# Optimization experiments

Measured on AMD Instinct MI355X. Metric: run time of the kernel, lower is better.

## Reference

```python
import jax, jax.numpy as jnp
import numpy as np


def _lstm_bi(x, wih, whh, b):
    # x: [B,T,D]; wih: [2,D,4H]; whh: [2,H,4H]; b: [2,4H]. PyTorch gate order i,f,g,o.
    def run(xs, wi, wh, bb):
        B, H = xs.shape[1], wh.shape[0]
        def step(carry, xt):
            h, c = carry
            g = xt @ wi + h @ wh + bb
            i, f, gg, o = jnp.split(g, 4, axis=-1)
            c = jax.nn.sigmoid(f) * c + jax.nn.sigmoid(i) * jnp.tanh(gg)
            h = jax.nn.sigmoid(o) * jnp.tanh(c)
            return (h, c), h
        z0 = jnp.zeros((B, H), xs.dtype)
        _, hs = jax.lax.scan(step, (z0, z0), xs)
        return hs
    xs = jnp.swapaxes(x, 0, 1)  # [T,B,D]
    hf = run(xs, wih[0], whh[0], b[0])
    hb = run(xs[::-1], wih[1], whh[1], b[1])[::-1]
    return jnp.swapaxes(jnp.concatenate([hf, hb], axis=-1), 0, 1)


def _norm_thr(att, thr):
    # sum-normalize, threshold-sparsify, renormalize (PSP core)
    att = att / (jnp.sum(att, -1, keepdims=True) + 1e-8)
    att = jnp.where(att > thr, att, jnp.zeros_like(att))
    return att / (jnp.sum(att, -1, keepdims=True) + 1e-8)


def _ln(x, g, b):
    mu = jnp.mean(x, -1, keepdims=True)
    var = jnp.mean(jnp.square(x - mu), -1, keepdims=True)
    return (x - mu) / jnp.sqrt(var + 1e-6) * g + b


def _forward(audio, video, thr_val, fa_w1, fa_w2, av_aw, av_ab, av_vw, av_vb,
             av_v2w, av_gw, av_hw, fv_w1, fv_w2, la_wih, la_whh, la_b,
             lv_wih, lv_whh, lv_b, vL1, vL2, aL1, aL2, vfc, afc, ln_g, ln_b, L1w, L2w):
    bs, T = audio.shape[0], audio.shape[1]
    fa = (audio @ fa_w1) @ fa_w2                          # [B,T,128]
    vf = video.reshape(bs, T, -1, video.shape[-1])        # [B,T,49,512]
    # AVGA audio-guided visual attention
    v_h = jax.nn.relu(vf @ av_vw + av_vb)                 # [B,T,49,512]
    a_h = jax.nn.relu(fa @ av_aw + av_ab)                 # [B,T,512]
    content = v_h @ av_v2w + (a_h @ av_gw)[..., None]     # [B,T,49,49]
    z = jnp.squeeze(jnp.tanh(content) @ av_hw, -1)        # [B,T,49]
    alpha = jax.nn.softmax(z, -1)
    video_t = jnp.einsum('btp,btpd->btd', alpha, vf)      # [B,T,512]
    video_t = (video_t @ fv_w1) @ fv_w2                   # [B,T,128]
    # bidirectional LSTMs
    lstm_a = _lstm_bi(fa, la_wih, la_whh, la_b)           # [B,T,256]
    lstm_v = _lstm_bi(video_t, lv_wih, lv_whh, lv_b)      # [B,T,256]
    # PSP (eval mode: dropout is identity)
    v_b1 = jax.nn.relu(lstm_v @ vL1)
    v_b2 = jax.nn.relu(lstm_v @ vL2)
    a_b1 = jax.nn.relu(lstm_a @ aL1)
    a_b2 = jax.nn.relu(lstm_a @ aL2)
    scale = 1.0 / jnp.sqrt(jnp.asarray(v_b2.shape[-1], v_b2.dtype))
    att = jax.nn.relu(jnp.einsum('bvd,bad->bva', v_b2, a_b1) * scale)  # v->a raw
    att_v2a = _norm_thr(att, thr_val)
    att_a2v = _norm_thr(jnp.swapaxes(att, 1, 2), thr_val)
    v_psp = lstm_v + jnp.einsum('bva,bad->bvd', att_v2a, a_b2)
    a_psp = lstm_a + jnp.einsum('bav,bvd->bad', att_a2v, v_b1)
    v_psp = _ln(jax.nn.relu(v_psp @ vfc), ln_g, ln_b)
    a_psp = _ln(jax.nn.relu(a_psp @ afc), ln_g, ln_b)
    fuse = 0.5 * (v_psp + a_psp)
    vn = v_psp / jnp.maximum(jnp.linalg.norm(v_psp, axis=-1, keepdims=True), 1e-12)
    an = a_psp / jnp.maximum(jnp.linalg.norm(a_psp, axis=-1, keepdims=True), 1e-12)
    cross_att = jnp.sum(vn * an, -1)                      # [B,T]
    out = jax.nn.relu(fuse @ L1w) @ L2w                   # [B,T,29]
    return (fuse, out, cross_att)


def setup_inputs() -> dict:
    key = jax.random.key(0)
    ks = iter(jax.random.split(key, 40))
    def w(*shape):
        fan_in = shape[-2] if len(shape) > 1 else shape[-1]
        return jax.random.normal(next(ks), shape, jnp.float32) * (1.0 / np.sqrt(fan_in))
    B, T = 256, 10
    return dict(
        audio=jax.random.normal(next(ks), (B, T, 128), jnp.float32),
        video=jax.random.normal(next(ks), (B, T, 7, 7, 512), jnp.float32),
        thr_val=jnp.float32(0.099),
        fa_w1=w(128, 256), fa_w2=w(256, 128),
        av_aw=w(128, 512), av_ab=jnp.zeros((512,), jnp.float32),
        av_vw=w(512, 512), av_vb=jnp.zeros((512,), jnp.float32),
        av_v2w=w(512, 49), av_gw=w(512, 49), av_hw=w(49, 1),
        fv_w1=w(512, 256), fv_w2=w(256, 128),
        la_wih=w(2, 128, 512), la_whh=w(2, 128, 512), la_b=jnp.zeros((2, 512), jnp.float32),
        lv_wih=w(2, 128, 512), lv_whh=w(2, 128, 512), lv_b=jnp.zeros((2, 512), jnp.float32),
        vL1=w(256, 256), vL2=w(256, 256), aL1=w(256, 256), aL2=w(256, 256),
        vfc=w(256, 256), afc=w(256, 256),
        ln_g=jnp.ones((256,), jnp.float32), ln_b=jnp.zeros((256,), jnp.float32),
        L1w=w(256, 64), L2w=w(64, 29),
    )


def reference(audio, video, thr_val, fa_w1, fa_w2, av_aw, av_ab, av_vw, av_vb,
              av_v2w, av_gw, av_hw, fv_w1, fv_w2, la_wih, la_whh, la_b,
              lv_wih, lv_whh, lv_b, vL1, vL2, aL1, aL2, vfc, afc, ln_g, ln_b, L1w, L2w):
    return _forward(audio, video, thr_val, fa_w1, fa_w2, av_aw, av_ab, av_vw, av_vb,
                    av_v2w, av_gw, av_hw, fv_w1, fv_w2, la_wih, la_whh, la_b,
                    lv_wih, lv_whh, lv_b, vL1, vL2, aL1, aL2, vfc, afc, ln_g, ln_b, L1w, L2w)
```

## Files before the change

### kernel.cpp

```cpp
#include <hip/hip_runtime.h>
#include <math.h>

#define DEV __device__ __forceinline__

typedef _Float16 f16x8 __attribute__((ext_vector_type(8)));
typedef _Float16 f16x4 __attribute__((ext_vector_type(4)));
typedef float    f32x4 __attribute__((ext_vector_type(4)));

DEV float sigmoidf_(float x){ return 1.0f/(1.0f + expf(-x)); }

DEV float wred64(float x){
    #pragma unroll
    for (int off=32; off; off>>=1) x += __shfl_xor(x, off);
    return x;
}

#define MFMA16(a,b,c) __builtin_amdgcn_mfma_f32_16x16x32_f16(a,b,c,0,0,0)

DEV void packone(const float* __restrict__ src, int N, int NfrTot, int nfOff,
                 _Float16* __restrict__ Dh, _Float16* __restrict__ Dl, int o){
    int j = o&7, l16 = (o>>3)&15, kg = (o>>7)&3;
    int rest = o>>9;
    int nfl = rest % (N>>4), kt = rest / (N>>4);
    int k = kt*32 + kg*8 + j, n = nfl*16 + l16;
    float x = src[(size_t)k*N + n];
    _Float16 h = (_Float16)x;
    size_t d = ((size_t)kt*NfrTot + nfOff + nfl)*512 + kg*128 + l16*8 + j;
    Dh[d] = h; Dl[d] = (_Float16)(x - (float)h);
}

__global__ __launch_bounds__(256) void k_prep(
    const float* __restrict__ fa_w1, const float* __restrict__ fa_w2, float* __restrict__ faW,
    const float* __restrict__ fv_w1, const float* __restrict__ fv_w2,
    const float* __restrict__ av_vw, _Float16* __restrict__ Bh, _Float16* __restrict__ Bl,
    const float* __restrict__ v2w, _Float16* __restrict__ Wh, _Float16* __restrict__ Wl,
    const float* __restrict__ lv_wih,
    _Float16* __restrict__ PKfv_h, _Float16* __restrict__ PKfv_l,
    _Float16* __restrict__ PKxv_h, _Float16* __restrict__ PKxv_l)
{
    int bid = blockIdx.x, t = threadIdx.x;
    if (bid < 64){
        int idx = bid*256+t; int m = idx>>7, n = idx&127;
        float acc=0.f;
        for (int k=0;k<256;k++) acc += fa_w1[m*256+k]*fa_w2[k*128+n];
        faW[idx]=acc;
    } else if (bid < 1088){
        int o = (bid-64)*256+t;
        int j = o & 7, l16 = (o>>3)&15, kg = (o>>7)&3, nf = (o>>9)&31, kt = o>>14;
        int k = kt*32 + kg*8 + j, n = nf*16 + l16;
        float x = av_vw[(size_t)k*512 + n];
        _Float16 h = (_Float16)x;
        Bh[o] = h; Bl[o] = (_Float16)(x - (float)h);
    } else if (bid < 1216){
        int o = (bid-1088)*256+t;
        int j = o & 7, l16 = (o>>3)&15, kg = (o>>7)&3, qf = (o>>9)&3, kbg = o>>11;
        int k = kbg*32 + kg*8 + j, q = qf*16 + l16;
        float x = (q < 49) ? v2w[(size_t)k*49 + q] : 0.f;
        _Float16 h = (_Float16)x;
        Wh[o] = h; Wl[o] = (_Float16)(x - (float)h);
    } else if (bid < 1472){
        int o = (bid-1216)*256+t;
        int j=o&7, l16=(o>>3)&15, kg=(o>>7)&3; int rest=o>>9;
        int nfl = rest&7, kt = rest>>3;
        int k = kt*32+kg*8+j, n = nfl*16+l16;
        float acc=0.f;
        for (int kk=0;kk<256;kk++) acc += fv_w1[k*256+kk]*fv_w2[kk*128+n];
        _Float16 h=(_Float16)acc;
        size_t d = ((size_t)kt*8 + nfl)*512 + kg*128 + l16*8 + j;
        PKfv_h[d]=h; PKfv_l[d]=(_Float16)(acc-(float)h);
    } else {
        int seg = (bid-1472)>>8;
        int o = ((bid-1472)&255)*256+t;
        packone(lv_wih + (size_t)seg*65536, 512, 64, seg*32, PKxv_h, PKxv_l, o);
    }
}

__global__ __launch_bounds__(512) void k_faga2(
    const float* __restrict__ audio, const float* __restrict__ faW,
    const float* __restrict__ av_aw, const float* __restrict__ av_ab,
    const float* __restrict__ av_gw,
    const float* __restrict__ la_wih, const float* __restrict__ la_b,
    float* __restrict__ gGA, float* __restrict__ xpA)
{
    int b0 = blockIdx.x*8; int tid = threadIdx.x;
    __shared__ float sau[8][128], sfa[8][128], sah[8][512];
    for (int i=tid;i<1024;i+=512){ int bt=i>>7,k=i&127; sau[bt][k]=audio[(size_t)(b0+bt)*128+k]; }
    __syncthreads();
    for (int u=0;u<2;u++){
        int i=tid+u*512, bt=i>>7, n=i&127;
        float acc=0.f;
        for (int k4=0;k4<32;k4++){
            float4 x4=*(const float4*)&sau[bt][k4*4];
            acc+=x4.x*faW[(k4*4)*128+n]+x4.y*faW[(k4*4+1)*128+n]
                +x4.z*faW[(k4*4+2)*128+n]+x4.w*faW[(k4*4+3)*128+n];
        }
        sfa[bt][n]=acc;
    }
    __syncthreads();
    {
        int n=tid;
        float bv=av_ab[n];
        float acc[8]={bv,bv,bv,bv,bv,bv,bv,bv};
        for (int k4=0;k4<32;k4++){
            float w0=av_aw[(k4*4)*512+n], w1=av_aw[(k4*4+1)*512+n],
                  w2=av_aw[(k4*4+2)*512+n], w3=av_aw[(k4*4+3)*512+n];
            #pragma unroll
            for (int bt=0;bt<8;bt++){
                float4 x4=*(const float4*)&sfa[bt][k4*4];
                acc[bt]+=x4.x*w0+x4.y*w1+x4.z*w2+x4.w*w3;
            }
        }
        #pragma unroll
        for (int bt=0;bt<8;bt++) sah[bt][n]=fmaxf(acc[bt],0.f);
    }
    __syncthreads();
    if (tid<392){
        int bt=tid/49, q=tid%49;
        float acc=0.f;
        for (int k=0;k<512;k++) acc+=sah[bt][k]*av_gw[k*49+q];
        gGA[(size_t)(b0+bt)*49+q]=acc;
    }
    for (int u=0;u<2;u++){
        int n = tid + u*512;
        int dir = n >> 9, g = n & 511;
        const float* W = la_wih + (size_t)dir*65536;
        float bvv = la_b[dir*512 + g];
        float acc[8] = {bvv,bvv,bvv,bvv,bvv,bvv,bvv,bvv};
        for (int k4=0;k4<32;k4++){
            float w0=W[(k4*4+0)*512+g], w1=W[(k4*4+1)*512+g],
                  w2=W[(k4*4+2)*512+g], w3=W[(k4*4+3)*512+g];
            #pragma unroll
            for (int bt=0;bt<8;bt++){
                float4 x4=*(const float4*)&sfa[bt][k4*4];
                acc[bt]+=x4.x*w0+x4.y*w1+x4.z*w2+x4.w*w3;
            }
        }
        #pragma unroll
        for (int bt=0;bt<8;bt++)
            xpA[((size_t)(b0+bt))*1024 + n] = acc[bt];
    }
}

DEV void cvt4_(float4 v, f16x4& hv, f16x4& lv){
    hv[0]=(_Float16)v.x; lv[0]=(_Float16)(v.x-(float)hv[0]);
    hv[1]=(_Float16)v.y; lv[1]=(_Float16)(v.y-(float)hv[1]);
    hv[2]=(_Float16)v.z; lv[2]=(_Float16)(v.z-(float)hv[2]);
    hv[3]=(_Float16)v.w; lv[3]=(_Float16)(v.w-(float)hv[3]);
}

__global__ __launch_bounds__(256,2) void k_avga_fused(
    const float* __restrict__ video,
    const _Float16* __restrict__ Bh, const _Float16* __restrict__ Bl,
    const float* __restrict__ bias,
    const _Float16* __restrict__ Wh, const _Float16* __restrict__ Wl,
    const float* __restrict__ gGA, const float* __restrict__ hw,
    float* __restrict__ vT)
{
    __shared__ __align__(16) char smem[67072];
    int bt = blockIdx.x;
    int t = threadIdx.x;
    int lane = t & 63, w = t >> 6;
    int l16 = lane & 15, lq = lane >> 4;
    int lb = lane * 16;

    int am = t >> 3, ak = (t & 7) * 4;
    int aoff1 = ((am>>4)*4 + (ak>>3))*256 + (am&15)*16 + (ak&7)*2;
    int am2 = am + 32;
    int aoff2 = ((am2>>4)*4 + (ak>>3))*256 + (am2&15)*16 + (ak&7)*2;
    size_t r1 = (size_t)bt*49 + am;  if (r1 > 125439) r1 = 125439;
    size_t r2 = (size_t)bt*49 + am2; if (r2 > 125439) r2 = 125439;
    const float* Arow1 = video + r1*512 + ak;
    const float* Arow2 = video + r2*512 + ak;

    const f32x4 vzero = {0.f,0.f,0.f,0.f};
    f32x4 acc[4][8];
    #pragma unroll
    for (int p=0;p<4;p++)
        #pragma unroll
        for (int q=0;q<8;q++) acc[p][q] = vzero;

    float4 pa0, pa1;
    pa0 = *(const float4*)(Arow1);
    pa1 = *(const float4*)(Arow2);
    {
        f16x4 hv, lv;
        char* h = &smem[0];
        cvt4_(pa0, hv, lv);
        *(f16x4*)(h + aoff1) = hv; *(f16x4*)(h + 4096 + aoff1) = lv;
        cvt4_(pa1, hv, lv);
        *(f16x4*)(h + aoff2) = hv; *(f16x4*)(h + 4096 + aoff2) = lv;
    }
    __syncthreads();

    for (int kt = 0; kt < 16; ++kt){
        int cur = kt & 1;
        bool more = (kt < 15);
        if (more){
            pa0 = *(const float4*)(Arow1 + (kt+1)*32);
            pa1 = *(const float4*)(Arow2 + (kt+1)*32);
        }
        const char* aB = &smem[cur*8192];
        f16x8 ah[4], al[4];
        #pragma unroll
        for (int p=0;p<4;p++){
            ah[p] = *(const f16x8*)(aB + p*1024 + lb);
            al[p] = *(const f16x8*)(aB + 4096 + p*1024 + lb);
        }
        #pragma unroll
        for (int q=0;q<8;q++){
            size_t bo = (size_t)kt*16384 + (size_t)(w*8 + q)*512 + lane*8;
            f16x8 bh  = *(const f16x8*)(Bh + bo);
            f16x8 bl2 = *(const f16x8*)(Bl + bo);
            #pragma unroll
            for (int p=0;p<4;p++){
                acc[p][q] = MFMA16(ah[p], bh,  acc[p][q]);
                acc[p][q] = MFMA16(ah[p], bl2, acc[p][q]);
                acc[p][q] = MFMA16(al[p], bh,  acc[p][q]);
            }
        }
        if (more){
            char* h = &smem[(cur^1)*8192];
            f16x4 hv, lv;
            cvt4_(pa0, hv, lv);
            *(f16x4*)(h + aoff1) = hv; *(f16x4*)(h + 4096 + aoff1) = lv;
            cvt4_(pa1, hv, lv);
            *(f16x4*)(h + aoff2) = hv; *(f16x4*)(h + 4096 + aoff2) = lv;
        }
        __syncthreads();
    }

    float bv[8];
    #pragma unroll
    for (int q=0;q<8;q++) bv[q] = bias[w*128 + q*16 + l16];

    char* vh = &smem[16384 + w*8192];
    f32x4 cacc[4][4];
    #pragma unroll
    for (int p=0;p<4;p++)
        #pragma unroll
        for (int qf=0;qf<4;qf++) cacc[p][qf] = vzero;

    #pragma unroll
    for (int c=0;c<4;c++){
        #pragma unroll
        for (int p=0;p<4;p++)
            #pragma unroll
            for (int qq=0;qq<2;qq++){
                int q = c*2 + qq;
                int offbase = p*1024 + (qq*2 + (l16>>3))*256 + (l16&7)*2;
                #pragma unroll
                for (int r=0;r<4;r++){
                    float x = fmaxf(acc[p][q][r] + bv[q], 0.f);
                    _Float16 hh = (_Float16)x;
                    _Float16 ll = (_Float16)(x - (float)hh);
                    int off = offbase + (lq*4 + r)*16;
                    *(_Float16*)(vh + off)        = hh;
                    *(_Float16*)(vh + 4096 + off) = ll;
                }
            }
        int kbg = w*4 + c;
        f16x8 vhh[4], vhl[4];
        #pragma unroll
        for (int p=0;p<4;p++){
            vhh[p] = *(const f16x8*)(vh + p*1024 + lb);
            vhl[p] = *(const f16x8*)(vh + 4096 + p*1024 + lb);
        }
        #pragma unroll
        for (int qf=0;qf<4;qf++){
            size_t wo = (size_t)kbg*2048 + qf*512 + lane*8;
            f16x8 wh = *(const f16x8*)(Wh + wo);
            f16x8 wl = *(const f16x8*)(Wl + wo);
            #pragma unroll
            for (int p=0;p<4;p++){
                cacc[p][qf] = MFMA16(vhh[p], wh, cacc[p][qf]);
                cacc[p][qf] = MFMA16(vhh[p], wl, cacc[p][qf]);
                cacc[p][qf] = MFMA16(vhl[p], wh, cacc[p][qf]);
            }
        }
    }

    __syncthreads();
    float* pw = (float*)&smem[w*16384];
    #pragma unroll
    for (int p=0;p<4;p++)
        #pragma unroll
        for (int qf=0;qf<4;qf++)
            #pragma unroll
            for (int r=0;r<4;r++)
                pw[(p*16 + lq*4 + r)*64 + qf*16 + l16] = cacc[p][qf][r];
    __syncthreads();
    float* cb = (float*)&smem[0];
    for (int i=t; i<4096; i+=256)
        cb[i] = cb[i] + cb[4096+i] + cb[8192+i] + cb[12288+i];
    __syncthreads();

    float* szp    = (float*)&smem[65536];
    float* salpha = (float*)&smem[66560];
    if (t < 196){
        int p = t >> 2, ds = t & 3;
        float ga = gGA[(size_t)bt*49 + p];
        float part = 0.f;
        for (int q = ds*13; q < ds*13+13 && q < 49; q++)
            part += tanhf(cb[p*64 + q] + ga) * hw[q];
        szp[t] = part;
    }
    __syncthreads();
    if (t < 64){
        float z = (t<49) ? (szp[t*4]+szp[t*4+1]+szp[t*4+2]+szp[t*4+3]) : -1e30f;
        float m = z;
        #pragma unroll
        for (int off=32; off; off>>=1) m = fmaxf(m, __shfl_xor(m, off));
        float e = (t<49)? expf(z - m) : 0.f;
        float s = e;
        #pragma unroll
        for (int off=32; off; off>>=1) s += __shfl_xor(s, off);
        salpha[t] = e / s;
    }
    __syncthreads();
    const float* vb = video + (size_t)bt*49*512;
    #pragma unroll
    for (int u=0;u<2;u++){
        int d = t + u*256;
        float a0 = 0.f;
        for (int p=0;p<49;p++) a0 += salpha[p] * vb[(size_t)p*512 + d];
        vT[(size_t)bt*512 + d] = a0;
    }
}

__global__ __launch_bounds__(256) void k_gemm2(
    const float* __restrict__ vT,
    const _Float16* __restrict__ Fh, const _Float16* __restrict__ Fl,
    const _Float16* __restrict__ Xh, const _Float16* __restrict__ Xl,
    const float* __restrict__ lv_b,
    float* __restrict__ xpV)
{
    __shared__ __align__(16) char sA[2][4096];
    __shared__ float sV[32][132];
    int t = threadIdx.x, lane = t&63, w = t>>6;
    int l16 = lane&15, lq = lane>>4, lb = lane*16;
    int row0 = blockIdx.x * 32;

    int am = t>>3, ak = (t&7)*4;
    int aoff = ((am>>4)*4 + (ak>>3))*256 + (am&15)*16 + (ak&7)*2;
    const float* Arow = vT + (size_t)(row0+am)*512 + ak;

    const f32x4 vzero = {0.f,0.f,0.f,0.f};
    f32x4 acc1[2][2];
    #pragma unroll
    for (int p=0;p<2;p++)
        #pragma unroll
        for (int q=0;q<2;q++) acc1[p][q] = vzero;

    float4 pa = *(const float4*)(Arow);
    {
        f16x4 hv, lv;
        char* h = &sA[0][0];
        cvt4_(pa, hv, lv);
        *(f16x4*)(h + aoff) = hv; *(f16x4*)(h + 2048 + aoff) = lv;
    }
    __syncthreads();
    for (int kt = 0; kt < 16; ++kt){
        int cur = kt & 1;
        bool more = (kt < 15);
        if (more) pa = *(const float4*)(Arow + (kt+1)*32);
        const char* aB = &sA[cur][0];
        f16x8 ah[2], al[2];
        #pragma unroll
        for (int p=0;p<2;p++){
            ah[p] = *(const f16x8*)(aB + p*1024 + lb);
            al[p] = *(const f16x8*)(aB + 2048 + p*1024 + lb);
        }
        #pragma unroll
        for (int q=0;q<2;q++){
            size_t bo = ((size_t)kt*8 + w*2 + q)*512 + lane*8;
            f16x8 bh  = *(const f16x8*)(Fh + bo);
            f16x8 bl2 = *(const f16x8*)(Fl + bo);
            #pragma unroll
            for (int p=0;p<2;p++){
                acc1[p][q] = MFMA16(ah[p], bh,  acc1[p][q]);
                acc1[p][q] = MFMA16(ah[p], bl2, acc1[p][q]);
                acc1[p][q] = MFMA16(al[p], bh,  acc1[p][q]);
            }
        }
        if (more){
            char* h = &sA[cur^1][0];
            f16x4 hv, lv;
            cvt4_(pa, hv, lv);
            *(f16x4*)(h + aoff) = hv; *(f16x4*)(h + 2048 + aoff) = lv;
        }
        __syncthreads();
    }
    #pragma unroll
    for (int q=0;q<2;q++){
        int n = (w*2+q)*16 + l16;
        #pragma unroll
        for (int p=0;p<2;p++)
            #pragma unroll
            for (int r=0;r<4;r++)
                sV[p*16 + lq*4 + r][n] = acc1[p][q][r];
    }
    __syncthreads();

    int nf0 = blockIdx.y*16 + w*4;
    f32x4 acc2[2][4];
    #pragma unroll
    for (int p=0;p<2;p++)
        #pragma unroll
        for (int q=0;q<4;q++) acc2[p][q] = vzero;

    pa = *(const float4*)&sV[am][ak];
    {
        f16x4 hv, lv;
        char* h = &sA[0][0];
        cvt4_(pa, hv, lv);
        *(f16x4*)(h + aoff) = hv; *(f16x4*)(h + 2048 + aoff) = lv;
    }
    __syncthreads();
    for (int kt = 0; kt < 4; ++kt){
        int cur = kt & 1;
        bool more = (kt < 3);
        if (more) pa = *(const float4*)&sV[am][(kt+1)*32 + ak];
        const char* aB = &sA[cur][0];
        f16x8 ah[2], al[2];
        #pragma unroll
        for (int p=0;p<2;p++){
            ah[p] = *(const f16x8*)(aB + p*1024 + lb);
            al[p] = *(const f16x8*)(aB + 2048 + p*1024 + lb);
        }
        #pragma unroll
        for (int q=0;q<4;q++){
            size_t bo = ((size_t)kt*64 + nf0 + q)*512 + lane*8;
            f16x8 bh  = *(const f16x8*)(Xh + bo);
            f16x8 bl2 = *(const f16x8*)(Xl + bo);
            #pragma unroll
            for (int p=0;p<2;p++){
                acc2[p][q] = MFMA16(ah[p], bh,  acc2[p][q]);
                acc2[p][q] = MFMA16(ah[p], bl2, acc2[p][q]);
                acc2[p][q] = MFMA16(al[p], bh,  acc2[p][q]);
            }
        }
        if (more){
            char* h = &sA[cur^1][0];
            f16x4 hv, lv;
            cvt4_(pa, hv, lv);
            *(f16x4*)(h + aoff) = hv; *(f16x4*)(h + 2048 + aoff) = lv;
        }
        __syncthreads();
    }
    #pragma unroll
    for (int q=0;q<4;q++){
        int n = (nf0+q)*16 + l16;
        float bv = lv_b[n];
        #pragma unroll
        for (int p=0;p<2;p++){
            #pragma unroll
            for (int r=0;r<4;r++)
                xpV[(size_t)(row0 + p*16 + lq*4 + r)*1024 + n] = acc2[p][q][r] + bv;
        }
    }
}

__global__ __launch_bounds__(512) void k_lstm(
    const float* __restrict__ xpA, const float* __restrict__ xpV,
    const float* __restrict__ la_whh, const float* __restrict__ lv_whh,
    float* __restrict__ lstm_a, float* __restrict__ lstm_v)
{
    int blk = blockIdx.x;
    int c = blk >> 6;
    int chunk = blk & 63;
    int tid = threadIdx.x;
    int j  = tid & 127;
    int bh = (tid >> 7) & 1;
    int kh = tid >> 8;
    const float* whh = ((c<2)? la_whh : lv_whh) + (size_t)(c&1)*65536;
    const float* xpm = (c<2)? xpA : xpV;
    float* outp = (c<2)? lstm_a : lstm_v;
    int dir = c & 1;

    __shared__ float hbuf[4][128];
    __shared__ float pg[4][4][128];
    float cc[2] = {0.f,0.f};
    if (tid < 512) { if (tid < 512 && tid < 512) {} }
    for (int i=tid;i<512;i+=512) ((float*)hbuf)[i] = 0.f;
    __syncthreads();

    for (int s=0; s<10; s++){
        int tt = dir ? (9-s) : s;
        float gi[2]={0.f,0.f}, gf[2]={0.f,0.f}, gg[2]={0.f,0.f}, go[2]={0.f,0.f};
        int k0 = kh*64;
        #pragma unroll 4
        for (int k=k0;k<k0+64;k++){
            float wi = whh[k*512 + j];
            float wf = whh[k*512 + 128 + j];
            float wg = whh[k*512 + 256 + j];
            float wo = whh[k*512 + 384 + j];
            #pragma unroll
            for (int b=0;b<2;b++){
                float hk = hbuf[bh*2+b][k];
                gi[b] += hk*wi; gf[b] += hk*wf; gg[b] += hk*wg; go[b] += hk*wo;
            }
        }
        if (kh==1){
            #pragma unroll
            for (int b=0;b<2;b++){
                int sp = bh*2+b;
                pg[sp][0][j]=gi[b]; pg[sp][1][j]=gf[b];
                pg[sp][2][j]=gg[b]; pg[sp][3][j]=go[b];
            }
        }
        __syncthreads();
        if (kh==0){
            #pragma unroll
            for (int b=0;b<2;b++){
                int gb = chunk*4 + bh*2 + b;
                int sp = bh*2+b;
                const float* xrow = xpm + ((size_t)gb*10 + tt)*1024 + dir*512;
                float gi_ = xrow[j]       + gi[b] + pg[sp][0][j];
                float gf_ = xrow[128+j]   + gf[b] + pg[sp][1][j];
                float gg_ = xrow[256+j]   + gg[b] + pg[sp][2][j];
                float go_ = xrow[384+j]   + go[b] + pg[sp][3][j];
                float i_ = sigmoidf_(gi_);
                float f_ = sigmoidf_(gf_);
                float g_ = tanhf(gg_);
                float o_ = sigmoidf_(go_);
                cc[b] = f_*cc[b] + i_*g_;
                float h_ = o_*tanhf(cc[b]);
                hbuf[sp][j] = h_;
                outp[((size_t)gb*10 + tt)*256 + dir*128 + j] = h_;
            }
        }
        __syncthreads();
    }
}

__global__ __launch_bounds__(512) void k_tail(
    const float* __restrict__ lstm_a, const float* __restrict__ lstm_v,
    const float* __restrict__ vL1, const float* __restrict__ vL2,
    const float* __restrict__ aL1, const float* __restrict__ aL2,
    const float* __restrict__ vfc, const float* __restrict__ afc,
    const float* __restrict__ thrp,
    const float* __restrict__ ln_g, const float* __restrict__ ln_b,
    const float* __restrict__ L1w, const float* __restrict__ L2w,
    float* __restrict__ dout)
{
    int b = blockIdx.x, tid = threadIdx.x;
    int t = tid & 255;
    int half = tid >> 8;
    int lane = tid & 63, w = tid >> 6;
    int wl = w & 3;
    int r0 = half*5;

    __shared__ float sla[10][256], slv[10][256];
    __shared__ float sb1v[10][256], sb2v[10][256], sb1a[10][256], sb2a[10][256];
    __shared__ float sfu[10][256];
    __shared__ float s64[10][64];
    __shared__ float satt[100], s_v2a[100], s_a2v[100];
    __shared__ float sredp[10][4][4];
    __shared__ float scos[10][3][4];

    size_t base = (size_t)b*2560;
    for (int i=tid;i<2560;i+=512){
        ((float*)sla)[i] = lstm_a[base+i];
        ((float*)slv)[i] = lstm_v[base+i];
    }
    __syncthreads();

    {
        float a1[5], a2[5];
        #pragma unroll
        for (int r=0;r<5;r++){ a1[r]=0.f; a2[r]=0.f; }
        #pragma unroll 4
        for (int k=0;k<256;k++){
            float w1 = vL1[k*256+t], w2 = vL2[k*256+t];
            #pragma unroll
            for (int r=0;r<5;r++){ float x=slv[r0+r][k]; a1[r]+=x*w1; a2[r]+=x*w2; }
        }
        #pragma unroll
        for (int r=0;r<5;r++){ sb1v[r0+r][t]=fmaxf(a1[r],0.f); sb2v[r0+r][t]=fmaxf(a2[r],0.f); }
        #pragma unroll
        for (int r=0;r<5;r++){ a1[r]=0.f; a2[r]=0.f; }
        #pragma unroll 4
        for (int k=0;k<256;k++){
            float w1 = aL1[k*256+t], w2 = aL2[k*256+t];
            #pragma unroll
            for (int r=0;r<5;r++){ float x=sla[r0+r][k]; a1[r]+=x*w1; a2[r]+=x*w2; }
        }
        #pragma unroll
        for (int r=0;r<5;r++){ sb1a[r0+r][t]=fmaxf(a1[r],0.f); sb2a[r0+r][t]=fmaxf(a2[r],0.f); }
    }
    __syncthreads();

    if (tid < 100){
        int v = tid/10, a = tid - v*10;
        float acc=0.f;
        for (int k=0;k<256;k++) acc += sb2v[v][k]*sb1a[a][k];
        satt[tid] = fmaxf(acc*(1.0f/16.0f), 0.f);
    }
    __syncthreads();
    float thr = thrp[0];
    if (tid < 10){
        int v = tid;
        float rs=0.f; for(int a=0;a<10;a++) rs += satt[v*10+a];
        float inv = 1.f/(rs+1e-8f);
        float tmp[10]; float rs2=0.f;
        for(int a=0;a<10;a++){ float x = satt[v*10+a]*inv; x = (x>thr)?x:0.f; tmp[a]=x; rs2+=x; }
        float inv2 = 1.f/(rs2+1e-8f);
        for(int a=0;a<10;a++) s_v2a[v*10+a] = tmp[a]*inv2;
    } else if (tid>=16 && tid<26){
        int a = tid-16;
        float cs=0.f; for(int v=0;v<10;v++) cs += satt[v*10+a];
        float inv = 1.f/(cs+1e-8f);
        float tmp[10]; float cs2=0.f;
        for(int v=0;v<10;v++){ float x = satt[v*10+a]*inv; x=(x>thr)?x:0.f; tmp[v]=x; cs2+=x; }
        float inv2 = 1.f/(cs2+1e-8f);
        for(int v=0;v<10;v++) s_a2v[a*10+v] = tmp[v]*inv2;
    }
    __syncthreads();

    #pragma unroll
    for (int v=0;v<5;v++){
        int row = r0+v;
        float acc = slv[row][t];
        #pragma unroll
        for (int a=0;a<10;a++) acc += s_v2a[row*10+a]*sb2a[a][t];
        slv[row][t] = acc;
    }
    #pragma unroll
    for (int a=0;a<5;a++){
        int row = r0+a;
        float acc = sla[row][t];
        #pragma unroll
        for (int v=0;v<10;v++) acc += s_a2v[row*10+v]*sb1v[v][t];
        sla[row][t] = acc;
    }
    __syncthreads();

    float fv[5], fa2[5];
    #pragma unroll
    for (int r=0;r<5;r++){ fv[r]=0.f; fa2[r]=0.f; }
    #pragma unroll 4
    for (int k=0;k<256;k++){
        float wv = vfc[k*256+t], wa = afc[k*256+t];
        #pragma unroll
        for (int r=0;r<5;r++){ fv[r]+=slv[r0+r][k]*wv; fa2[r]+=sla[r0+r][k]*wa; }
    }
    #pragma unroll
    for (int r=0;r<5;r++){ fv[r]=fmaxf(fv[r],0.f); fa2[r]=fmaxf(fa2[r],0.f); }

    #pragma unroll
    for (int r=0;r<5;r++){
        float s1 = wred64(fv[r]);
        float s2 = wred64(fv[r]*fv[r]);
        float s3 = wred64(fa2[r]);
        float s4 = wred64(fa2[r]*fa2[r]);
        if (lane==0){
            sredp[r0+r][0][wl] = s1; sredp[r0+r][1][wl] = s2;
            sredp[r0+r][2][wl] = s3; sredp[r0+r][3][wl] = s4;
        }
    }
    __syncthreads();
    float gt = ln_g[t], bt2 = ln_b[t];
    #pragma unroll
    for (int r=0;r<5;r++){
        int row = r0+r;
        float s1 = sredp[row][0][0]+sredp[row][0][1]+sredp[row][0][2]+sredp[row][0][3];
        float s2 = sredp[row][1][0]+sredp[row][1][1]+sredp[row][1][2]+sredp[row][1][3];
        float s3 = sredp[row][2][0]+sredp[row][2][1]+sredp[row][2][2]+sredp[row][2][3];
        float s4 = sredp[row][3][0]+sredp[row][3][1]+sredp[row][3][2]+sredp[row][3][3];
        float muv = s1*(1.f/256.f);
        float varv = s2*(1.f/256.f) - muv*muv;
        float rsv = 1.f/sqrtf(varv+1e-6f);
        float vln = (fv[r]-muv)*rsv*gt + bt2;
        float mua = s3*(1.f/256.f);
        float vara = s4*(1.f/256.f) - mua*mua;
        float rsa = 1.f/sqrtf(vara+1e-6f);
        float aln = (fa2[r]-mua)*rsa*gt + bt2;
        float fu = 0.5f*(vln+aln);
        dout[(size_t)(b*10+row)*256 + t] = fu;
        sfu[row][t] = fu;
        float c1 = wred64(vln*vln);
        float c2 = wred64(aln*aln);
        float c3 = wred64(vln*aln);
        if (lane==0){
            scos[row][0][wl] = c1; scos[row][1][wl] = c2; scos[row][2][wl] = c3;
        }
    }
    __syncthreads();
    if (tid < 10){
        int r = tid;
        float nv2 = scos[r][0][0]+scos[r][0][1]+scos[r][0][2]+scos[r][0][3];
        float na2 = scos[r][1][0]+scos[r][1][1]+scos[r][1][2]+scos[r][1][3];
        float dva = scos[r][2][0]+scos[r][2][1]+scos[r][2][2]+scos[r][2][3];
        float nv = fmaxf(sqrtf(nv2), 1e-12f);
        float na = fmaxf(sqrtf(na2), 1e-12f);
        dout[729600 + b*10 + r] = dva/(nv*na);
    }

    #pragma unroll
    for (int pass=0; pass<2; ++pass){
        int r = pass*8 + w;
        if (r < 10){
            float acc = 0.f;
            for (int k4=0;k4<64;k4++){
                float4 f4 = *(const float4*)&sfu[r][k4*4];
                acc += f4.x*L1w[(k4*4)*64+lane] + f4.y*L1w[(k4*4+1)*64+lane]
                     + f4.z*L1w[(k4*4+2)*64+lane] + f4.w*L1w[(k4*4+3)*64+lane];
            }
            s64[r][lane] = fmaxf(acc, 0.f);
        }
    }
    __syncthreads();
    for (int i=tid; i<290; i+=512){
        int r = i/29, jj = i - r*29;
        float acc = 0.f;
        #pragma unroll
        for (int k=0;k<64;k++) acc += s64[r][k]*L2w[k*29+jj];
        dout[655360 + (size_t)(b*10+r)*29 + jj] = acc;
    }
}

extern "C" void kernel_launch(void* const* d_in, const int* in_sizes, int n_in,
                              void* d_out, int out_size, void* d_ws, size_t ws_size,
                              hipStream_t stream) {
    const float* audio  = (const float*)d_in[0];
    const float* video  = (const float*)d_in[1];
    const float* thrp   = (const float*)d_in[2];
    const float* fa_w1  = (const float*)d_in[3];
    const float* fa_w2  = (const float*)d_in[4];
    const float* av_aw  = (const float*)d_in[5];
    const float* av_ab  = (const float*)d_in[6];
    const float* av_vw  = (const float*)d_in[7];
    const float* av_vb  = (const float*)d_in[8];
    const float* av_v2w = (const float*)d_in[9];
    const float* av_gw  = (const float*)d_in[10];
    const float* av_hw  = (const float*)d_in[11];
    const float* fv_w1  = (const float*)d_in[12];
    const float* fv_w2  = (const float*)d_in[13];
    const float* la_wih = (const float*)d_in[14];
    const float* la_whh = (const float*)d_in[15];
    const float* la_b   = (const float*)d_in[16];
    const float* lv_wih = (const float*)d_in[17];
    const float* lv_whh = (const float*)d_in[18];
    const float* lv_b   = (const float*)d_in[19];
    const float* vL1    = (const float*)d_in[20];
    const float* vL2    = (const float*)d_in[21];
    const float* aL1    = (const float*)d_in[22];
    const float* aL2    = (const float*)d_in[23];
    const float* vfc    = (const float*)d_in[24];
    const float* afc    = (const float*)d_in[25];
    const float* ln_g   = (const float*)d_in[26];
    const float* ln_b   = (const float*)d_in[27];
    const float* L1w    = (const float*)d_in[28];
    const float* L2w    = (const float*)d_in[29];
    float* dout = (float*)d_out;
    float* ws = (float*)d_ws;

    float* faW  = ws;
    float* gGA  = ws + 409600;
    float* vT   = ws + 535040;
    float* xpA  = ws + 2173440;
    float* xpV  = ws + 4794880;
    float* la   = ws + 7416320;
    float* lv   = ws + 8071680;
    _Float16* Bh = (_Float16*)(ws + 12659200);
    _Float16* Bl = (_Float16*)(ws + 12790272);
    _Float16* Wh = (_Float16*)(ws + 12921344);
    _Float16* Wl = (_Float16*)(ws + 12937728);
    _Float16* PKfv_h = (_Float16*)(ws + 12954112);
    _Float16* PKfv_l = (_Float16*)(ws + 12986880);
    _Float16* PKxv_h = (_Float16*)(ws + 13150720);
    _Float16* PKxv_l = (_Float16*)(ws + 13216256);

    k_prep<<<1984, 256, 0, stream>>>(fa_w1, fa_w2, faW, fv_w1, fv_w2,
                                     av_vw, Bh, Bl, av_v2w, Wh, Wl,
                                     lv_wih, PKfv_h, PKfv_l, PKxv_h, PKxv_l);
    k_faga2<<<320, 512, 0, stream>>>(audio, faW, av_aw, av_ab, av_gw,
                                     la_wih, la_b, gGA, xpA);
    k_avga_fused<<<2560, 256, 0, stream>>>(video, Bh, Bl, av_vb, Wh, Wl,
                                           gGA, av_hw, vT);
    k_gemm2<<<dim3(80,4), 256, 0, stream>>>(vT, PKfv_h, PKfv_l,
                                            PKxv_h, PKxv_l, lv_b, xpV);
    k_lstm<<<256, 512, 0, stream>>>(xpA, xpV, la_whh, lv_whh, la, lv);
    k_tail<<<256, 512, 0, stream>>>(la, lv, vL1, vL2, aL1, aL2, vfc, afc,
                                    thrp, ln_g, ln_b, L1w, L2w, dout);
}
```

Before: 604.3 us.

## Run audio LSTM inside AVGA kernel; spread video LSTM over more blocks

The audio bidirectional LSTM moves into extra blocks of the AVGA fused kernel, so it overlaps with the large video attention GEMM instead of running after it. The remaining video LSTM kernel now uses 256 blocks of 2 batch rows each, not 4 rows per block, which raises parallelism on the serial recurrence. The risk is that the added LSTM blocks use the large shared-memory footprint and launch bounds of the AVGA kernel, which may lower its occupancy. They also run a full 128-long k loop per thread, which could stretch the AVGA kernel's critical path.

```diff
diff --git a/kernel.cpp b/kernel.cpp
--- a/kernel.cpp
+++ b/kernel.cpp
@@ -154,11 +154,64 @@
     const float* __restrict__ bias,
     const _Float16* __restrict__ Wh, const _Float16* __restrict__ Wl,
     const float* __restrict__ gGA, const float* __restrict__ hw,
-    float* __restrict__ vT)
+    float* __restrict__ vT,
+    const float* __restrict__ xpA, const float* __restrict__ la_whh,
+    float* __restrict__ lstm_a)
 {
     __shared__ __align__(16) char smem[67072];
-    int bt = blockIdx.x;
     int t = threadIdx.x;
+
+    if (blockIdx.x < 128){
+        int blk2 = blockIdx.x;
+        int c = blk2 >> 6;
+        int chunk = blk2 & 63;
+        int j = t & 127, bh = t >> 7;
+        const float* whh = la_whh + (size_t)c*65536;
+        int dir = c;
+        float* hbuf = (float*)&smem[0];
+        float cc[2] = {0.f,0.f};
+        for (int i=t;i<512;i+=256) hbuf[i] = 0.f;
+        __syncthreads();
+        for (int s=0; s<10; s++){
+            int tt = dir ? (9-s) : s;
+            float gi[2], gf[2], gg[2], go[2];
+            #pragma unroll
+            for (int b=0;b<2;b++){
+                int gb = chunk*4 + bh*2 + b;
+                const float* xrow = xpA + ((size_t)gb*10 + tt)*1024 + dir*512;
+                gi[b]=xrow[j]; gf[b]=xrow[128+j]; gg[b]=xrow[256+j]; go[b]=xrow[384+j];
+            }
+            #pragma unroll 4
+            for (int k=0;k<128;k++){
+                float wi = whh[k*512 + j];
+                float wf = whh[k*512 + 128 + j];
+                float wg = whh[k*512 + 256 + j];
+                float wo = whh[k*512 + 384 + j];
+                #pragma unroll
+                for (int b=0;b<2;b++){
+                    float hk = hbuf[(bh*2+b)*128 + k];
+                    gi[b] += hk*wi; gf[b] += hk*wf; gg[b] += hk*wg; go[b] += hk*wo;
+                }
+            }
+            __syncthreads();
+            #pragma unroll
+            for (int b=0;b<2;b++){
+                float i_ = sigmoidf_(gi[b]);
+                float f_ = sigmoidf_(gf[b]);
+                float g_ = tanhf(gg[b]);
+                float o_ = sigmoidf_(go[b]);
+                cc[b] = f_*cc[b] + i_*g_;
+                float h_ = o_*tanhf(cc[b]);
+                hbuf[(bh*2+b)*128 + j] = h_;
+                int gb = chunk*4 + bh*2 + b;
+                lstm_a[((size_t)gb*10 + tt)*256 + dir*128 + j] = h_;
+            }
+            __syncthreads();
+        }
+        return;
+    }
+
+    int bt = blockIdx.x - 128;
     int lane = t & 63, w = t >> 6;
     int l16 = lane & 15, lq = lane >> 4;
     int lb = lane * 16;
@@ -461,73 +514,56 @@
 }
 
 __global__ __launch_bounds__(512) void k_lstm(
-    const float* __restrict__ xpA, const float* __restrict__ xpV,
-    const float* __restrict__ la_whh, const float* __restrict__ lv_whh,
-    float* __restrict__ lstm_a, float* __restrict__ lstm_v)
+    const float* __restrict__ xpV, const float* __restrict__ lv_whh,
+    float* __restrict__ lstm_v)
 {
     int blk = blockIdx.x;
-    int c = blk >> 6;
-    int chunk = blk & 63;
+    int dir = blk >> 7;
+    int chunk = blk & 127;
     int tid = threadIdx.x;
     int j  = tid & 127;
     int bh = (tid >> 7) & 1;
     int kh = tid >> 8;
-    const float* whh = ((c<2)? la_whh : lv_whh) + (size_t)(c&1)*65536;
-    const float* xpm = (c<2)? xpA : xpV;
-    float* outp = (c<2)? lstm_a : lstm_v;
-    int dir = c & 1;
-
-    __shared__ float hbuf[4][128];
-    __shared__ float pg[4][4][128];
-    float cc[2] = {0.f,0.f};
-    if (tid < 512) { if (tid < 512 && tid < 512) {} }
-    for (int i=tid;i<512;i+=512) ((float*)hbuf)[i] = 0.f;
+    const float* whh = lv_whh + (size_t)dir*65536;
+
+    __shared__ float hbuf[2][128];
+    __shared__ float pg[2][4][128];
+    float cc = 0.f;
+    for (int i=tid;i<256;i+=512) ((float*)hbuf)[i] = 0.f;
     __syncthreads();
 
     for (int s=0; s<10; s++){
         int tt = dir ? (9-s) : s;
-        float gi[2]={0.f,0.f}, gf[2]={0.f,0.f}, gg[2]={0.f,0.f}, go[2]={0.f,0.f};
+        float gi=0.f, gf=0.f, gg=0.f, go=0.f;
         int k0 = kh*64;
         #pragma unroll 4
         for (int k=k0;k<k0+64;k++){
-            float wi = whh[k*512 + j];
-            float wf = whh[k*512 + 128 + j];
-            float wg = whh[k*512 + 256 + j];
-            float wo = whh[k*512 + 384 + j];
-            #pragma unroll
-            for (int b=0;b<2;b++){
-                float hk = hbuf[bh*2+b][k];
-                gi[b] += hk*wi; gf[b] += hk*wf; gg[b] += hk*wg; go[b] += hk*wo;
-            }
+            float hk = hbuf[bh][k];
+            gi += hk*whh[k*512 + j];
+            gf += hk*whh[k*512 + 128 + j];
+            gg += hk*whh[k*512 + 256 + j];
+            go += hk*whh[k*512 + 384 + j];
         }
         if (kh==1){
-            #pragma unroll
-            for (int b=0;b<2;b++){
-                int sp = bh*2+b;
-                pg[sp][0][j]=gi[b]; pg[sp][1][j]=gf[b];
-                pg[sp][2][j]=gg[b]; pg[sp][3][j]=go[b];
-            }
+            pg[bh][0][j]=gi; pg[bh][1][j]=gf;
+            pg[bh][2][j]=gg; pg[bh][3][j]=go;
         }
         __syncthreads();
         if (kh==0){
-            #pragma unroll
-            for (int b=0;b<2;b++){
-                int gb = chunk*4 + bh*2 + b;
-                int sp = bh*2+b;
-                const float* xrow = xpm + ((size_t)gb*10 + tt)*1024 + dir*512;
-                float gi_ = xrow[j]       + gi[b] + pg[sp][0][j];
-                float gf_ = xrow[128+j]   + gf[b] + pg[sp][1][j];
-                float gg_ = xrow[256+j]   + gg[b] + pg[sp][2][j];
-                float go_ = xrow[384+j]   + go[b] + pg[sp][3][j];
-                float i_ = sigmoidf_(gi_);
-                float f_ = sigmoidf_(gf_);
-                float g_ = tanhf(gg_);
-                float o_ = sigmoidf_(go_);
-                cc[b] = f_*cc[b] + i_*g_;
-                float h_ = o_*tanhf(cc[b]);
-                hbuf[sp][j] = h_;
-                outp[((size_t)gb*10 + tt)*256 + dir*128 + j] = h_;
-            }
+            int gb = chunk*2 + bh;
+            const float* xrow = xpV + ((size_t)gb*10 + tt)*1024 + dir*512;
+            float gi_ = xrow[j]     + gi + pg[bh][0][j];
+            float gf_ = xrow[128+j] + gf + pg[bh][1][j];
+            float gg_ = xrow[256+j] + gg + pg[bh][2][j];
+            float go_ = xrow[384+j] + go + pg[bh][3][j];
+            float i_ = sigmoidf_(gi_);
+            float f_ = sigmoidf_(gf_);
+            float g_ = tanhf(gg_);
+            float o_ = sigmoidf_(go_);
+            cc = f_*cc + i_*g_;
+            float h_ = o_*tanhf(cc);
+            hbuf[bh][j] = h_;
+            lstm_v[((size_t)gb*10 + tt)*256 + dir*128 + j] = h_;
         }
         __syncthreads();
     }
@@ -776,11 +812,11 @@
                                      lv_wih, PKfv_h, PKfv_l, PKxv_h, PKxv_l);
     k_faga2<<<320, 512, 0, stream>>>(audio, faW, av_aw, av_ab, av_gw,
                                      la_wih, la_b, gGA, xpA);
-    k_avga_fused<<<2560, 256, 0, stream>>>(video, Bh, Bl, av_vb, Wh, Wl,
-                                           gGA, av_hw, vT);
+    k_avga_fused<<<2688, 256, 0, stream>>>(video, Bh, Bl, av_vb, Wh, Wl,
+                                           gGA, av_hw, vT, xpA, la_whh, la);
     k_gemm2<<<dim3(80,4), 256, 0, stream>>>(vT, PKfv_h, PKfv_l,
                                             PKxv_h, PKxv_l, lv_b, xpV);
-    k_lstm<<<256, 512, 0, stream>>>(xpA, xpV, la_whh, lv_whh, la, lv);
+    k_lstm<<<256, 512, 0, stream>>>(xpV, lv_whh, lv);
     k_tail<<<256, 512, 0, stream>>>(la, lv, vL1, vL2, aL1, aL2, vfc, afc,
                                     thrp, ln_g, ln_b, L1w, L2w, dout);
 }
```

Measured after the change: 638.7 us. 1.06x slower.
